# Kernel optimization log

Measured on AMD Instinct MI355X. Metric: run time of the kernel, lower is better.

## Reference

```python
import jax, jax.numpy as jnp
import numpy as np

N_NODES = 100_000
N_EDGES = 3_200_000
F_IN, F_HID, F_OUT = 128, 128, 64
BN_EPS = 1e-5


def gcn_conv(x, src, dst, W, b, n_nodes):
    """PyG GCNConv: x' = D^{-1/2}(A+I)D^{-1/2} (x W) + b, self-loops included in src/dst."""
    h = x @ W                                                  # [N, out]
    ones = jnp.ones(src.shape[0], dtype=x.dtype)
    deg = jax.ops.segment_sum(ones, dst, num_segments=n_nodes)  # in-degree incl. self-loop (>=1)
    dinv = jax.lax.rsqrt(deg)
    norm = dinv[src] * dinv[dst]                               # [E+N]
    msg = h[src] * norm[:, None]                               # gather + scale
    out = jax.ops.segment_sum(msg, dst, num_segments=n_nodes)  # scatter-add
    return out + b


def setup_inputs() -> dict:
    key = jax.random.key(0)
    ks = jax.random.split(key, 6)
    x = jax.random.normal(ks[0], (N_NODES, F_IN), dtype=jnp.float32)
    edge_index = jax.random.randint(ks[1], (2, N_EDGES), 0, N_NODES, dtype=jnp.int32)
    W1 = jax.random.normal(ks[2], (F_IN, F_HID), dtype=jnp.float32) / np.sqrt(F_IN)
    b1 = jnp.zeros((F_HID,), dtype=jnp.float32)
    gamma = jnp.ones((F_HID,), dtype=jnp.float32)
    beta = jnp.zeros((F_HID,), dtype=jnp.float32)
    W2 = jax.random.normal(ks[3], (F_HID, F_OUT), dtype=jnp.float32) / np.sqrt(F_HID)
    b2 = jnp.zeros((F_OUT,), dtype=jnp.float32)
    return {"x": x, "edge_index": edge_index, "W1": W1, "b1": b1,
            "gamma": gamma, "beta": beta, "W2": W2, "b2": b2}


def reference(x, edge_index, W1, b1, gamma, beta, W2, b2):
    n = x.shape[0]
    loop = jnp.arange(n, dtype=edge_index.dtype)
    src = jnp.concatenate([edge_index[0], loop])
    dst = jnp.concatenate([edge_index[1], loop])
    # conv1
    h = gcn_conv(x, src, dst, W1, b1, n)
    # BatchNorm1d (training mode: batch stats, biased variance)
    mean = jnp.mean(h, axis=0)
    var = jnp.mean((h - mean) ** 2, axis=0)
    h = (h - mean) * jax.lax.rsqrt(var + BN_EPS) * gamma + beta
    # ReLU
    h = jax.nn.relu(h)
    # conv2
    return gcn_conv(h, src, dst, W2, b2, n)
```

## Files before the change

kernel.cpp:

```cpp
#include <hip/hip_runtime.h>
#include <math.h>


typedef _Float16 f16;
typedef _Float16 f16x2 __attribute__((ext_vector_type(2)));
typedef _Float16 f16x8 __attribute__((ext_vector_type(8)));
typedef float f32x4 __attribute__((ext_vector_type(4)));

static constexpr int KDIM = 128;
static constexpr int MAXNB = 1600;
static constexpr int CAP = 2560;
static constexpr int CHUNK = 8192;
static constexpr int BINT = 512;
static constexpr int WTP = 136;

__global__ __launch_bounds__(BINT) void binA_kernel(
    const int* __restrict__ src, const int* __restrict__ dst, int E,
    int* __restrict__ bcur, unsigned int* __restrict__ bins, int nbuck) {
  __shared__ int hist[MAXNB];
  __shared__ int base[MAXNB];
  const int tid = threadIdx.x;
  for (int b = tid; b < nbuck; b += BINT) hist[b] = 0;
  __syncthreads();
  const int e0 = blockIdx.x * CHUNK;
  const int e1 = min(e0 + CHUNK, E);
  for (int e = e0 + tid; e < e1; e += BINT) atomicAdd(&hist[dst[e] >> 6], 1);
  __syncthreads();
  for (int b = tid; b < nbuck; b += BINT) {
    int c = hist[b];
    base[b] = c ? atomicAdd(&bcur[b], c) : 0;
    hist[b] = 0;
  }
  __syncthreads();
  for (int e = e0 + tid; e < e1; e += BINT) {
    int d = dst[e];
    int b = d >> 6;
    int lp = atomicAdd(&hist[b], 1);
    int p = base[b] + lp;
    if (p < CAP)
      bins[(size_t)b * CAP + p] = (unsigned int)src[e] | ((unsigned int)(d & 63) << 17);
  }
}

__global__ __launch_bounds__(1024) void bscan_kernel(
    const int* __restrict__ bcur, int nbuck, int* __restrict__ bbase,
    int* __restrict__ off_n, f16* __restrict__ h1rown) {
  __shared__ int sh[1024];
  const int t = threadIdx.x;
  if (t < 128) h1rown[t] = (f16)0.f;
  int a = (2 * t < nbuck) ? min(bcur[2 * t], CAP) : 0;
  int b = (2 * t + 1 < nbuck) ? min(bcur[2 * t + 1], CAP) : 0;
  sh[t] = a + b;
  __syncthreads();
  for (int o = 1; o < 1024; o <<= 1) {
    int v = (t >= o) ? sh[t - o] : 0;
    __syncthreads();
    sh[t] += v;
    __syncthreads();
  }
  int excl = (t > 0) ? sh[t - 1] : 0;
  if (2 * t < nbuck) bbase[2 * t] = excl;
  if (2 * t + 1 < nbuck) bbase[2 * t + 1] = excl + a;
  if (t == 1023) off_n[0] = sh[1023];
}

__global__ __launch_bounds__(256) void csrfill_kernel(
    const unsigned int* __restrict__ bins, const int* __restrict__ bcur,
    const int* __restrict__ bbase, int* __restrict__ csr, int* __restrict__ off,
    float* __restrict__ dinv, int n) {
  __shared__ int hist[64];
  __shared__ int pref[64];
  __shared__ int lcur[64];
  const int tid = threadIdx.x;
  const int b = blockIdx.x;
  const int cnt = min(bcur[b], CAP);
  const unsigned int* bp = bins + (size_t)b * CAP;
  if (tid < 64) hist[tid] = 0;
  __syncthreads();
  for (int e = tid; e < cnt; e += 256) atomicAdd(&hist[bp[e] >> 17], 1);
  __syncthreads();
  if (tid < 64) pref[tid] = hist[tid];
  __syncthreads();
  for (int o = 1; o < 64; o <<= 1) {
    int v = (tid < 64 && tid >= o) ? pref[tid - o] : 0;
    __syncthreads();
    if (tid < 64) pref[tid] += v;
    __syncthreads();
  }
  if (tid < 64) {
    int node = b * 64 + tid;
    if (node < n) {
      int excl = bbase[b] + pref[tid] - hist[tid];
      off[node] = excl;
      lcur[tid] = excl;
      dinv[node] = rsqrtf((float)(hist[tid] + 1));
    }
  }
  __syncthreads();
  for (int e = tid; e < cnt; e += 256) {
    unsigned int pk = bp[e];
    int r = pk >> 17;
    int p = atomicAdd(&lcur[r], 1);
    csr[p] = (int)(pk & 0x1FFFF);
  }
}

__global__ __launch_bounds__(256) void gemm1_kernel(
    const float* __restrict__ A, const float* __restrict__ W, f16* __restrict__ C,
    int M, const float* __restrict__ dinv) {
  __shared__ f16 Wt[128][WTP];
  const int tid = threadIdx.x;
  for (int idx = tid; idx < 128 * 128; idx += 256) {
    int k = idx >> 7, nn = idx & 127;
    Wt[nn][k] = (f16)W[idx];
  }
  __syncthreads();
  const int wave = tid >> 6;
  const int lane = tid & 63;
  const int r = lane & 15;
  const int kg = lane >> 4;
  const int row0 = blockIdx.x * 64 + wave * 16;
  const bool valid = (row0 + r) < M;
  const float* arow = A + (size_t)(row0 + r) * KDIM;
  f32x4 acc[8];
#pragma unroll
  for (int nf = 0; nf < 8; ++nf) acc[nf] = (f32x4){0.f, 0.f, 0.f, 0.f};
#pragma unroll
  for (int ks = 0; ks < 4; ++ks) {
    const int k0 = ks * 32 + kg * 8;
    f16x8 a;
#pragma unroll
    for (int z = 0; z < 8; ++z) a[z] = (f16)0.f;
    if (valid) {
      float4 u = *reinterpret_cast<const float4*>(arow + k0);
      float4 v = *reinterpret_cast<const float4*>(arow + k0 + 4);
      a[0] = (f16)u.x; a[1] = (f16)u.y; a[2] = (f16)u.z; a[3] = (f16)u.w;
      a[4] = (f16)v.x; a[5] = (f16)v.y; a[6] = (f16)v.z; a[7] = (f16)v.w;
    }
#pragma unroll
    for (int nf = 0; nf < 8; ++nf) {
      f16x8 b = *reinterpret_cast<const f16x8*>(&Wt[nf * 16 + r][k0]);
      acc[nf] = __builtin_amdgcn_mfma_f32_16x16x32_f16(a, b, acc[nf], 0, 0, 0);
    }
  }
  const int crow = row0 + (lane >> 4) * 4;
  const int ccol = lane & 15;
#pragma unroll
  for (int q = 0; q < 4; ++q) {
    int rr = crow + q;
    if (rr < M) {
      float dv = dinv[rr];
#pragma unroll
      for (int nf = 0; nf < 8; ++nf)
        C[(size_t)rr * 128 + nf * 16 + ccol] = (f16)(acc[nf][q] * dv);
    }
  }
}

__global__ __launch_bounds__(256) void gemm2_kernel(
    const f16* __restrict__ A, const float* __restrict__ W, f16* __restrict__ C,
    int M, const float* __restrict__ ss, const float* __restrict__ dinv) {
  __shared__ f16 Wt[64][WTP];
  const int tid = threadIdx.x;
  for (int idx = tid; idx < 128 * 64; idx += 256) {
    int k = idx >> 6, nn = idx & 63;
    Wt[nn][k] = (f16)W[idx];
  }
  __syncthreads();
  const int wave = tid >> 6;
  const int lane = tid & 63;
  const int r = lane & 15;
  const int kg = lane >> 4;
  const int row0 = blockIdx.x * 64 + wave * 16;
  const bool valid = (row0 + r) < M;
  const f16* arow = A + (size_t)(row0 + r) * KDIM;
  f32x4 acc[4];
#pragma unroll
  for (int nf = 0; nf < 4; ++nf) acc[nf] = (f32x4){0.f, 0.f, 0.f, 0.f};
#pragma unroll
  for (int ks = 0; ks < 4; ++ks) {
    const int k0 = ks * 32 + kg * 8;
    f16x8 a;
#pragma unroll
    for (int z = 0; z < 8; ++z) a[z] = (f16)0.f;
    if (valid) {
      f16x8 raw = *reinterpret_cast<const f16x8*>(arow + k0);
      float4 s0 = *reinterpret_cast<const float4*>(&ss[k0]);
      float4 s1 = *reinterpret_cast<const float4*>(&ss[k0 + 4]);
      float4 t0 = *reinterpret_cast<const float4*>(&ss[128 + k0]);
      float4 t1 = *reinterpret_cast<const float4*>(&ss[128 + k0 + 4]);
      a[0] = (f16)fmaxf((float)raw[0] * s0.x + t0.x, 0.f);
      a[1] = (f16)fmaxf((float)raw[1] * s0.y + t0.y, 0.f);
      a[2] = (f16)fmaxf((float)raw[2] * s0.z + t0.z, 0.f);
      a[3] = (f16)fmaxf((float)raw[3] * s0.w + t0.w, 0.f);
      a[4] = (f16)fmaxf((float)raw[4] * s1.x + t1.x, 0.f);
      a[5] = (f16)fmaxf((float)raw[5] * s1.y + t1.y, 0.f);
      a[6] = (f16)fmaxf((float)raw[6] * s1.z + t1.z, 0.f);
      a[7] = (f16)fmaxf((float)raw[7] * s1.w + t1.w, 0.f);
    }
#pragma unroll
    for (int nf = 0; nf < 4; ++nf) {
      f16x8 b = *reinterpret_cast<const f16x8*>(&Wt[nf * 16 + r][k0]);
      acc[nf] = __builtin_amdgcn_mfma_f32_16x16x32_f16(a, b, acc[nf], 0, 0, 0);
    }
  }
  const int crow = row0 + (lane >> 4) * 4;
  const int ccol = lane & 15;
#pragma unroll
  for (int q = 0; q < 4; ++q) {
    int rr = crow + q;
    if (rr < M) {
      float dv = dinv[rr];
#pragma unroll
      for (int nf = 0; nf < 4; ++nf)
        C[(size_t)rr * 64 + nf * 16 + ccol] = (f16)(acc[nf][q] * dv);
    }
  }
}

__global__ __launch_bounds__(64) void agg1_kernel(
    const f16* __restrict__ h, const float* __restrict__ dinv,
    const int* __restrict__ off, const int* __restrict__ csr,
    const float* __restrict__ bias, f16* __restrict__ outh, int n) {
  const int i = blockIdx.x;
  const int t = threadIdx.x;
  const float di = dinv[i];
  const float2 bi = *reinterpret_cast<const float2*>(&bias[2 * t]);
  f16x2 hs = *reinterpret_cast<const f16x2*>(&h[(size_t)i * 128 + 2 * t]);
  float e0 = (float)hs[0];
  float e1 = (float)hs[1];
  const int beg = __builtin_amdgcn_readfirstlane(off[i]);
  const int end = __builtin_amdgcn_readfirstlane(off[i + 1]);
  for (int j = beg & ~15; j < end; j += 16) {
    int4 q0 = *reinterpret_cast<const int4*>(&csr[j]);
    int4 q1 = *reinterpret_cast<const int4*>(&csr[j + 4]);
    int4 q2 = *reinterpret_cast<const int4*>(&csr[j + 8]);
    int4 q3 = *reinterpret_cast<const int4*>(&csr[j + 12]);
    int s[16] = {q0.x, q0.y, q0.z, q0.w, q1.x, q1.y, q1.z, q1.w,
                 q2.x, q2.y, q2.z, q2.w, q3.x, q3.y, q3.z, q3.w};
    if (j < beg || j + 16 > end) {
#pragma unroll
      for (int k = 0; k < 16; ++k)
        if (j + k < beg || j + k >= end) s[k] = n;
    }
    f16x2 v[16];
#pragma unroll
    for (int k = 0; k < 16; ++k)
      v[k] = *reinterpret_cast<const f16x2*>(&h[(size_t)s[k] * 128 + 2 * t]);
#pragma unroll
    for (int k = 0; k < 16; ++k) {
      e0 += (float)v[k][0];
      e1 += (float)v[k][1];
    }
  }
  f16x2 o;
  o[0] = (f16)(di * e0 + bi.x);
  o[1] = (f16)(di * e1 + bi.y);
  *reinterpret_cast<f16x2*>(&outh[(size_t)i * 128 + 2 * t]) = o;
}

__global__ __launch_bounds__(64) void agg2_kernel(
    const f16* __restrict__ h, const float* __restrict__ dinv,
    const int* __restrict__ off, const int* __restrict__ csr,
    const float* __restrict__ bias, float* __restrict__ out, int n) {
  const int i = blockIdx.x;
  const int t = threadIdx.x;
  const float di = dinv[i];
  float e = (float)h[(size_t)i * 64 + t];
  const int beg = __builtin_amdgcn_readfirstlane(off[i]);
  const int end = __builtin_amdgcn_readfirstlane(off[i + 1]);
  for (int j = beg & ~15; j < end; j += 16) {
    int4 q0 = *reinterpret_cast<const int4*>(&csr[j]);
    int4 q1 = *reinterpret_cast<const int4*>(&csr[j + 4]);
    int4 q2 = *reinterpret_cast<const int4*>(&csr[j + 8]);
    int4 q3 = *reinterpret_cast<const int4*>(&csr[j + 12]);
    int s[16] = {q0.x, q0.y, q0.z, q0.w, q1.x, q1.y, q1.z, q1.w,
                 q2.x, q2.y, q2.z, q2.w, q3.x, q3.y, q3.z, q3.w};
    if (j < beg || j + 16 > end) {
#pragma unroll
      for (int k = 0; k < 16; ++k)
        if (j + k < beg || j + k >= end) s[k] = n;
    }
    f16 v[16];
#pragma unroll
    for (int k = 0; k < 16; ++k) v[k] = h[(size_t)s[k] * 64 + t];
#pragma unroll
    for (int k = 0; k < 16; ++k) e += (float)v[k];
  }
  out[(size_t)i * 64 + t] = di * e + bias[t];
}

__global__ void bnstat_kernel(const f16* __restrict__ a, int n, float* __restrict__ acc) {
  const int c = threadIdx.x & 127;
  const int half = threadIdx.x >> 7;
  const int rstart = blockIdx.x * 2 + half;
  const int rstep = gridDim.x * 2;
  float s = 0.f, ss = 0.f;
  for (int r = rstart; r < n; r += rstep) {
    float v = (float)a[(size_t)r * 128 + c];
    s += v;
    ss += v * v;
  }
  atomicAdd(&acc[c], s);
  atomicAdd(&acc[128 + c], ss);
}

__global__ void bnfin_kernel(const float* __restrict__ acc, const float* __restrict__ gamma,
                             const float* __restrict__ beta, int n, float* __restrict__ ss,
                             f16* __restrict__ h2rown) {
  const int c = threadIdx.x;
  if (c < 64) h2rown[c] = (f16)0.f;
  const float inv_n = 1.f / (float)n;
  const float mean = acc[c] * inv_n;
  const float var = acc[128 + c] * inv_n - mean * mean;
  const float sc = gamma[c] * rsqrtf(var + 1e-5f);
  ss[c] = sc;
  ss[128 + c] = beta[c] - mean * sc;
}

extern "C" void kernel_launch(void* const* d_in, const int* in_sizes, int n_in,
                              void* d_out, int out_size, void* d_ws, size_t ws_size,
                              hipStream_t stream) {
  const float* x = (const float*)d_in[0];
  const int* ei = (const int*)d_in[1];
  const float* W1 = (const float*)d_in[2];
  const float* b1 = (const float*)d_in[3];
  const float* gamma = (const float*)d_in[4];
  const float* beta = (const float*)d_in[5];
  const float* W2 = (const float*)d_in[6];
  const float* b2 = (const float*)d_in[7];
  float* out = (float*)d_out;

  const int n = in_sizes[0] / 128;
  const int E = in_sizes[1] / 2;
  const int* src = ei;
  const int* dst = ei + E;
  const int nbuck = (n + 63) / 64;

  char* p = (char*)d_ws;
  auto carve = [&](size_t bytes) {
    char* r = p;
    p += (bytes + 255) & ~(size_t)255;
    return r;
  };
  int* bcur = (int*)carve((size_t)nbuck * 4);
  float* bnacc = (float*)carve(256 * 4);
  const size_t zero_bytes = (size_t)((char*)(bnacc + 256) - (char*)bcur);
  int* bbase = (int*)carve((size_t)(nbuck + 1) * 4);
  float* bnss = (float*)carve(256 * 4);
  int* off = (int*)carve((size_t)(n + 1) * 4);
  float* dinv = (float*)carve((size_t)n * 4);
  unsigned int* bins = (unsigned int*)carve((size_t)nbuck * CAP * 4);
  int* csr = (int*)carve((size_t)(E + 64) * 4);
  f16* h1 = (f16*)carve((size_t)(n + 1) * 128 * 2);
  f16* agg1 = (f16*)carve((size_t)n * 128 * 2);
  f16* h2 = h1;

  hipMemsetAsync(bcur, 0, zero_bytes, stream);

  const int ngb = (n + 63) / 64;

  binA_kernel<<<(E + CHUNK - 1) / CHUNK, BINT, 0, stream>>>(src, dst, E, bcur, bins, nbuck);
  bscan_kernel<<<1, 1024, 0, stream>>>(bcur, nbuck, bbase, off + n, h1 + (size_t)n * 128);
  csrfill_kernel<<<nbuck, 256, 0, stream>>>(bins, bcur, bbase, csr, off, dinv, n);

  gemm1_kernel<<<ngb, 256, 0, stream>>>(x, W1, h1, n, dinv);
  agg1_kernel<<<n, 64, 0, stream>>>(h1, dinv, off, csr, b1, agg1, n);

  bnstat_kernel<<<512, 256, 0, stream>>>(agg1, n, bnacc);
  bnfin_kernel<<<1, 128, 0, stream>>>(bnacc, gamma, beta, n, bnss, h2 + (size_t)n * 64);

  gemm2_kernel<<<ngb, 256, 0, stream>>>(agg1, W2, h2, n, bnss, dinv);
  agg2_kernel<<<n, 64, 0, stream>>>(h2, dinv, off, csr, b2, out, n);
}
```

Before: 341.9 us.

## Vectorize edge binning loads, pair edges in agg2, and widen BN stat reads

The binning kernel now reads dst and src as int4 so each thread handles four edges per iteration, with a scalar tail loop for the remainder. agg2 splits the 64-lane wave into two halves that each take alternate edges and read f16x2 pairs, then combine through a cross-half shuffle; the self-loop term and bias are added once at the end and the output is written as float2. bnstat reads eight f16 values per thread and reduces partial sums in shared memory before issuing the atomics. These target narrow scalar memory accesses and atomic traffic, at the cost of the int4 loads assuming 16-byte aligned chunk starts and extra shuffle and shared-memory reduction work.

```diff
diff --git a/kernel.cpp b/kernel.cpp
--- a/kernel.cpp
+++ b/kernel.cpp
@@ -24,7 +24,14 @@
   __syncthreads();
   const int e0 = blockIdx.x * CHUNK;
   const int e1 = min(e0 + CHUNK, E);
-  for (int e = e0 + tid; e < e1; e += BINT) atomicAdd(&hist[dst[e] >> 6], 1);
+  for (int e = e0 + tid * 4; e + 3 < e1; e += BINT * 4) {
+    int4 d4 = *reinterpret_cast<const int4*>(&dst[e]);
+    atomicAdd(&hist[d4.x >> 6], 1);
+    atomicAdd(&hist[d4.y >> 6], 1);
+    atomicAdd(&hist[d4.z >> 6], 1);
+    atomicAdd(&hist[d4.w >> 6], 1);
+  }
+  for (int e = e1 - (e1 - e0) % 4 + tid; e < e1; e += BINT) atomicAdd(&hist[dst[e] >> 6], 1);
   __syncthreads();
   for (int b = tid; b < nbuck; b += BINT) {
     int c = hist[b];
@@ -32,7 +39,22 @@
     hist[b] = 0;
   }
   __syncthreads();
-  for (int e = e0 + tid; e < e1; e += BINT) {
+  for (int e = e0 + tid * 4; e + 3 < e1; e += BINT * 4) {
+    int4 d4 = *reinterpret_cast<const int4*>(&dst[e]);
+    int4 s4 = *reinterpret_cast<const int4*>(&src[e]);
+    int dd[4] = {d4.x, d4.y, d4.z, d4.w};
+    int ss[4] = {s4.x, s4.y, s4.z, s4.w};
+#pragma unroll
+    for (int k = 0; k < 4; ++k) {
+      int b = dd[k] >> 6;
+      int lp = atomicAdd(&hist[b], 1);
+      int p = base[b] + lp;
+      if (p < CAP)
+        bins[(size_t)b * CAP + p] =
+            (unsigned int)ss[k] | ((unsigned int)(dd[k] & 63) << 17);
+    }
+  }
+  for (int e = e1 - (e1 - e0) % 4 + tid; e < e1; e += BINT) {
     int d = dst[e];
     int b = d >> 6;
     int lp = atomicAdd(&hist[b], 1);
@@ -264,9 +286,11 @@
     const int* __restrict__ off, const int* __restrict__ csr,
     const float* __restrict__ bias, float* __restrict__ out, int n) {
   const int i = blockIdx.x;
-  const int t = threadIdx.x;
+  const int lane = threadIdx.x;
+  const int epar = lane >> 5;
+  const int cp = lane & 31;
   const float di = dinv[i];
-  float e = (float)h[(size_t)i * 64 + t];
+  float e0 = 0.f, e1 = 0.f;
   const int beg = __builtin_amdgcn_readfirstlane(off[i]);
   const int end = __builtin_amdgcn_readfirstlane(off[i + 1]);
   for (int j = beg & ~15; j < end; j += 16) {
@@ -281,28 +305,58 @@
       for (int k = 0; k < 16; ++k)
         if (j + k < beg || j + k >= end) s[k] = n;
     }
-    f16 v[16];
-#pragma unroll
-    for (int k = 0; k < 16; ++k) v[k] = h[(size_t)s[k] * 64 + t];
-#pragma unroll
-    for (int k = 0; k < 16; ++k) e += (float)v[k];
-  }
-  out[(size_t)i * 64 + t] = di * e + bias[t];
-}
-
-__global__ void bnstat_kernel(const f16* __restrict__ a, int n, float* __restrict__ acc) {
-  const int c = threadIdx.x & 127;
-  const int half = threadIdx.x >> 7;
-  const int rstart = blockIdx.x * 2 + half;
-  const int rstep = gridDim.x * 2;
-  float s = 0.f, ss = 0.f;
-  for (int r = rstart; r < n; r += rstep) {
-    float v = (float)a[(size_t)r * 128 + c];
-    s += v;
-    ss += v * v;
-  }
-  atomicAdd(&acc[c], s);
-  atomicAdd(&acc[128 + c], ss);
+#pragma unroll
+    for (int k = 0; k < 8; ++k) {
+      int se = epar ? s[2 * k + 1] : s[2 * k];
+      f16x2 v = *reinterpret_cast<const f16x2*>(&h[(size_t)se * 64 + 2 * cp]);
+      e0 += (float)v[0];
+      e1 += (float)v[1];
+    }
+  }
+  e0 += __shfl_xor(e0, 32, 64);
+  e1 += __shfl_xor(e1, 32, 64);
+  if (epar == 0) {
+    f16x2 hv = *reinterpret_cast<const f16x2*>(&h[(size_t)i * 64 + 2 * cp]);
+    float2 bi = *reinterpret_cast<const float2*>(&bias[2 * cp]);
+    float2 o;
+    o.x = di * (e0 + (float)hv[0]) + bi.x;
+    o.y = di * (e1 + (float)hv[1]) + bi.y;
+    *reinterpret_cast<float2*>(&out[(size_t)i * 64 + 2 * cp]) = o;
+  }
+}
+
+__global__ __launch_bounds__(256) void bnstat_kernel(
+    const f16* __restrict__ a, int n, float* __restrict__ acc) {
+  __shared__ float sh[16][16][16];
+  const int cgrp = threadIdx.x & 15;
+  const int rgrp = threadIdx.x >> 4;
+  float s[8], ss[8];
+#pragma unroll
+  for (int z = 0; z < 8; ++z) { s[z] = 0.f; ss[z] = 0.f; }
+  for (int r = blockIdx.x * 16 + rgrp; r < n; r += gridDim.x * 16) {
+    f16x8 v = *reinterpret_cast<const f16x8*>(&a[(size_t)r * 128 + cgrp * 8]);
+#pragma unroll
+    for (int z = 0; z < 8; ++z) {
+      float f = (float)v[z];
+      s[z] += f;
+      ss[z] += f * f;
+    }
+  }
+#pragma unroll
+  for (int z = 0; z < 8; ++z) {
+    sh[rgrp][cgrp][z] = s[z];
+    sh[rgrp][cgrp][8 + z] = ss[z];
+  }
+  __syncthreads();
+  const int cg = threadIdx.x >> 4;
+  const int zs = threadIdx.x & 15;
+  float tot = 0.f;
+#pragma unroll
+  for (int rg = 0; rg < 16; ++rg) tot += sh[rg][cg][zs];
+  if (zs < 8)
+    atomicAdd(&acc[cg * 8 + zs], tot);
+  else
+    atomicAdd(&acc[128 + cg * 8 + (zs - 8)], tot);
 }
 
 __global__ void bnfin_kernel(const float* __restrict__ acc, const float* __restrict__ gamma,
```

After: 302.2 us. 11.6% less time.
